# Performance work log

Measured on AMD Instinct MI355X. Metric: run time of the kernel, lower is better.

The kernel has to match this reference:

```python
import math
import jax, jax.numpy as jnp
import numpy as np

S, B, K, D, T, MAX_LEN = 2048, 128, 64, 256, 6, 2048
LOG_2PI = math.log(2.0 * math.pi)


def _make_pe(d_model, max_len):
    position = np.arange(max_len, dtype=np.float32)[:, None]
    div_term = np.exp(np.arange(0, d_model, 2, dtype=np.float32) * (-math.log(10000.0) / d_model))
    pe = np.zeros((max_len, 1, d_model), dtype=np.float32)
    pe[:, 0, 0::2] = np.sin(position * div_term)
    pe[:, 0, 1::2] = np.cos(position * div_term)  # d_model even
    return jnp.asarray(pe)


def setup_inputs() -> dict:
    key = jax.random.key(0)
    k1, k2, k3, k4, k5 = jax.random.split(key, 5)
    traj_feats = jax.random.normal(k1, (S, B, T), dtype=jnp.float32)
    xy_coords = jax.random.normal(k2, (S, B, 2), dtype=jnp.float32)
    means = jax.random.normal(k3, (K, 2), dtype=jnp.float32)          # key centers
    A = jax.random.normal(k4, (K, 2, 2), dtype=jnp.float32)          # PSD factor: cov = A A^T
    W = jax.random.normal(k5, (D, K), dtype=jnp.float32) * (1.0 / math.sqrt(K))  # Linear weight
    b = jnp.zeros((D,), dtype=jnp.float32)
    pe = _make_pe(D, MAX_LEN)
    return {"traj_feats": traj_feats, "xy_coords": xy_coords,
            "means": means, "A": A, "W": W, "b": b, "pe": pe}


def reference(traj_feats, xy_coords, means, A, W, b, pe):
    # Batched 2x2 Gaussian log-prob over all keys (fused, closed-form).
    cov = jnp.einsum('kij,klj->kil', A, A)                    # (K,2,2) = A A^T
    det = cov[:, 0, 0] * cov[:, 1, 1] - cov[:, 0, 1] * cov[:, 1, 0]  # (K,)
    inv = jnp.stack([
        jnp.stack([cov[:, 1, 1], -cov[:, 0, 1]], axis=-1),
        jnp.stack([-cov[:, 1, 0], cov[:, 0, 0]], axis=-1),
    ], axis=-2) / det[:, None, None]                          # (K,2,2)
    diff = xy_coords[:, :, None, :] - means                   # (S,B,K,2)
    quad = jnp.einsum('sbki,kij,sbkj->sbk', diff, inv, diff)  # Mahalanobis^2
    log_weights = -0.5 * (quad + jnp.log(det) + 2.0 * LOG_2PI)  # (S,B,K)
    # Weighted-sum embedding (Linear over key axis) + positional encoding.
    emb = jnp.einsum('sbk,dk->sbd', log_weights, W) + b       # (S,B,D)
    emb = emb + pe[:emb.shape[0]]                             # pe: (max_len,1,D)
    # dropout layers are identity at inference
    return jnp.concatenate([traj_feats, emb], axis=-1)        # (S,B,T+D)
```

## Files before the change

### kernel.cpp

```cpp
#include <hip/hip_runtime.h>
#include <math.h>

#define S_DIM 2048
#define B_DIM 128
#define K_DIM 64
#define D_DIM 256
#define T_DIM 6
#define ROW_LEN (T_DIM + D_DIM)
#define LOG_2PI_F 1.8378770664093453f
#define RPB 16

__global__ __launch_bounds__(256) void coef_kernel(
    const float* __restrict__ means,
    const float* __restrict__ A,
    const float* __restrict__ W,
    const float* __restrict__ bvec,
    float* __restrict__ Mt)
{
    __shared__ float c[6][K_DIM];
    int t = threadIdx.x;
    if (t < K_DIM) {
        float a00 = A[4*t+0], a01 = A[4*t+1], a10 = A[4*t+2], a11 = A[4*t+3];
        float cov00 = a00*a00 + a01*a01;
        float cov01 = a00*a10 + a01*a11;
        float cov11 = a10*a10 + a11*a11;
        float det   = cov00*cov11 - cov01*cov01;
        float rdet  = 1.0f / det;
        float i00 =  cov11*rdet, i01 = -cov01*rdet, i11 = cov00*rdet;
        float mx = means[2*t], my = means[2*t+1];
        c[0][t] = -0.5f*(i00*mx*mx + 2.0f*i01*mx*my + i11*my*my + logf(det)) - LOG_2PI_F;
        c[1][t] = i00*mx + i01*my;
        c[2][t] = i01*mx + i11*my;
        c[3][t] = -0.5f*i00;
        c[4][t] = -i01;
        c[5][t] = -0.5f*i11;
    }
    __syncthreads();
    int d = t;
    float m0 = 0.f, m1 = 0.f, m2 = 0.f, m3 = 0.f, m4 = 0.f, m5 = 0.f;
    const float* wrow = W + d*K_DIM;
#pragma unroll
    for (int k = 0; k < K_DIM; ++k) {
        float w = wrow[k];
        m0 += w*c[0][k]; m1 += w*c[1][k]; m2 += w*c[2][k];
        m3 += w*c[3][k]; m4 += w*c[4][k]; m5 += w*c[5][k];
    }
    Mt[0*D_DIM + d] = m0 + bvec[d];
    Mt[1*D_DIM + d] = m1;
    Mt[2*D_DIM + d] = m2;
    Mt[3*D_DIM + d] = m3;
    Mt[4*D_DIM + d] = m4;
    Mt[5*D_DIM + d] = m5;
}

__global__ __launch_bounds__(256) void emb_kernel(
    const float* __restrict__ traj,
    const float* __restrict__ xy,
    const float* __restrict__ pe,
    const float* __restrict__ Mt,
    float* __restrict__ out)
{
    __shared__ float tile[RPB * ROW_LEN];
    __shared__ float xys[2 * RPB];

    int t    = threadIdx.x;
    int blk  = blockIdx.x;
    int row0 = blk * RPB;
    int s    = row0 >> 7;

    if (t < 8) {
        float4 v = ((const float4*)xy)[blk * 8 + t];
        ((float4*)xys)[t] = v;
    }
    if (t >= 64 && t < 88) {
        int i = t - 64;
        float4 v = ((const float4*)traj)[blk * 24 + i];
        int j = i * 4;
        tile[(j    / T_DIM) * ROW_LEN + (j    % T_DIM)] = v.x;
        tile[((j+1)/ T_DIM) * ROW_LEN + ((j+1)% T_DIM)] = v.y;
        tile[((j+2)/ T_DIM) * ROW_LEN + ((j+2)% T_DIM)] = v.z;
        tile[((j+3)/ T_DIM) * ROW_LEN + ((j+3)% T_DIM)] = v.w;
    }

    float m0 = Mt[0*D_DIM + t] + pe[s*D_DIM + t];
    float m1 = Mt[1*D_DIM + t], m2 = Mt[2*D_DIM + t];
    float m3 = Mt[3*D_DIM + t], m4 = Mt[4*D_DIM + t], m5 = Mt[5*D_DIM + t];

    __syncthreads();

#pragma unroll
    for (int r = 0; r < RPB; ++r) {
        float x = xys[2*r], y = xys[2*r + 1];
        float v = m0 + m1*x + m2*y + (m3*x + m4*y)*x + m5*y*y;
        tile[r * ROW_LEN + T_DIM + t] = v;
    }

    __syncthreads();

    const float4* t4 = (const float4*)tile;
    float4* o4 = (float4*)(out + (size_t)row0 * ROW_LEN);
#pragma unroll
    for (int k = 0; k < 4; ++k)
        o4[k * 256 + t] = t4[k * 256 + t];
    if (t < 24)
        o4[1024 + t] = t4[1024 + t];
}

extern "C" void kernel_launch(void* const* d_in, const int* in_sizes, int n_in,
                              void* d_out, int out_size, void* d_ws, size_t ws_size,
                              hipStream_t stream) {
    const float* traj  = (const float*)d_in[0];
    const float* xy    = (const float*)d_in[1];
    const float* means = (const float*)d_in[2];
    const float* A     = (const float*)d_in[3];
    const float* W     = (const float*)d_in[4];
    const float* bvec  = (const float*)d_in[5];
    const float* pe    = (const float*)d_in[6];
    float* out = (float*)d_out;
    float* Mt  = (float*)d_ws;

    coef_kernel<<<1, 256, 0, stream>>>(means, A, W, bvec, Mt);

    int nrows = S_DIM * B_DIM;
    int grid  = nrows / RPB;
    emb_kernel<<<grid, 256, 0, stream>>>(traj, xy, pe, Mt, out);
}
```

Before: 296.6 us.

## Parallelize coefficient kernel across blocks, double rows per block, use nontemporal stores

The coefficient kernel now runs on 16 blocks. Each group of 16 lanes loads a float4 slice of a W row and reduces it with warp shuffles, replacing the single-block serial 64-step loop. The embedding kernel handles 32 rows per block instead of 16, which doubles the shared tile and halves the grid. Output writes use nontemporal stores so the large streaming output bypasses cache retention. The larger tile raises shared memory per block, which may reduce occupancy.

```diff
diff --git a/kernel.cpp b/kernel.cpp
--- a/kernel.cpp
+++ b/kernel.cpp
@@ -8,7 +8,9 @@
 #define T_DIM 6
 #define ROW_LEN (T_DIM + D_DIM)
 #define LOG_2PI_F 1.8378770664093453f
-#define RPB 16
+#define RPB 32
+
+typedef float v4f __attribute__((ext_vector_type(4)));
 
 __global__ __launch_bounds__(256) void coef_kernel(
     const float* __restrict__ means,
@@ -36,21 +38,27 @@
         c[5][t] = -0.5f*i11;
     }
     __syncthreads();
-    int d = t;
-    float m0 = 0.f, m1 = 0.f, m2 = 0.f, m3 = 0.f, m4 = 0.f, m5 = 0.f;
-    const float* wrow = W + d*K_DIM;
+
+    int d = blockIdx.x * 16 + (t >> 4);
+    int q = t & 15;
+    float4 w = ((const float4*)W)[blockIdx.x * 256 + t];
+
+    float m[6];
 #pragma unroll
-    for (int k = 0; k < K_DIM; ++k) {
-        float w = wrow[k];
-        m0 += w*c[0][k]; m1 += w*c[1][k]; m2 += w*c[2][k];
-        m3 += w*c[3][k]; m4 += w*c[4][k]; m5 += w*c[5][k];
+    for (int j = 0; j < 6; ++j) {
+        const float* cj = &c[j][4*q];
+        m[j] = w.x*cj[0] + w.y*cj[1] + w.z*cj[2] + w.w*cj[3];
+        m[j] += __shfl_xor(m[j], 1);
+        m[j] += __shfl_xor(m[j], 2);
+        m[j] += __shfl_xor(m[j], 4);
+        m[j] += __shfl_xor(m[j], 8);
     }
-    Mt[0*D_DIM + d] = m0 + bvec[d];
-    Mt[1*D_DIM + d] = m1;
-    Mt[2*D_DIM + d] = m2;
-    Mt[3*D_DIM + d] = m3;
-    Mt[4*D_DIM + d] = m4;
-    Mt[5*D_DIM + d] = m5;
+    if (q == 0) {
+        Mt[0*D_DIM + d] = m[0] + bvec[d];
+#pragma unroll
+        for (int j = 1; j < 6; ++j)
+            Mt[j*D_DIM + d] = m[j];
+    }
 }
 
 __global__ __launch_bounds__(256) void emb_kernel(
@@ -68,13 +76,13 @@
     int row0 = blk * RPB;
     int s    = row0 >> 7;
 
-    if (t < 8) {
-        float4 v = ((const float4*)xy)[blk * 8 + t];
+    if (t < 16) {
+        float4 v = ((const float4*)xy)[blk * 16 + t];
         ((float4*)xys)[t] = v;
     }
-    if (t >= 64 && t < 88) {
+    if (t >= 64 && t < 112) {
         int i = t - 64;
-        float4 v = ((const float4*)traj)[blk * 24 + i];
+        float4 v = ((const float4*)traj)[blk * 48 + i];
         int j = i * 4;
         tile[(j    / T_DIM) * ROW_LEN + (j    % T_DIM)] = v.x;
         tile[((j+1)/ T_DIM) * ROW_LEN + ((j+1)% T_DIM)] = v.y;
@@ -97,13 +105,13 @@
 
     __syncthreads();
 
-    const float4* t4 = (const float4*)tile;
-    float4* o4 = (float4*)(out + (size_t)row0 * ROW_LEN);
+    const v4f* t4 = (const v4f*)tile;
+    v4f* o4 = (v4f*)(out + (size_t)row0 * ROW_LEN);
 #pragma unroll
-    for (int k = 0; k < 4; ++k)
-        o4[k * 256 + t] = t4[k * 256 + t];
-    if (t < 24)
-        o4[1024 + t] = t4[1024 + t];
+    for (int k = 0; k < 8; ++k)
+        __builtin_nontemporal_store(t4[k * 256 + t], &o4[k * 256 + t]);
+    if (t < 48)
+        __builtin_nontemporal_store(t4[2048 + t], &o4[2048 + t]);
 }
 
 extern "C" void kernel_launch(void* const* d_in, const int* in_sizes, int n_in,
@@ -119,7 +127,7 @@
     float* out = (float*)d_out;
     float* Mt  = (float*)d_ws;
 
-    coef_kernel<<<1, 256, 0, stream>>>(means, A, W, bvec, Mt);
+    coef_kernel<<<16, 256, 0, stream>>>(means, A, W, bvec, Mt);
 
     int nrows = S_DIM * B_DIM;
     int grid  = nrows / RPB;
```

After: 293.0 us. Within noise of the previous version (-1.2%).
